# Performance work log

Measured on AMD Instinct MI355X. Metric: run time of the kernel, lower is better.

The kernel has to match this reference:

```python
import jax, jax.numpy as jnp
import numpy as np

P = 8          # patch_size = window_size // 3
C = 3          # in_channel (forced to 3 by the module's reshape logic)
QK_SCALE = 1.0


def _rel_bias(p):
    """Fixed relative-position bias [9, p, p], matching the torch constructor."""
    i = np.arange(p, dtype=np.float64)
    down = np.exp(-i / (p / 2))[:, None] * np.ones((1, p))   # down[i, :] = exp(-i/(p/2))
    right = down.T
    br = np.exp(-(i[:, None] + i[None, :]) / (p / 2))        # symmetric exp(-(i+j)/(p/2))
    merge = np.stack([
        np.rot90(br, 2), np.flip(down, 0), np.rot90(br, 1),
        np.flip(right, 1), np.ones((p, p)), right,
        np.rot90(br, 3), down, br,
    ], axis=0)
    return jnp.asarray(merge, dtype=jnp.float32)


def setup_inputs() -> dict:
    key = jax.random.key(0)
    k1, k2, k3 = jax.random.split(key, 3)
    b, c, h, w = 8, C, 512, 512
    d = c * P * P  # 192
    x = jax.random.normal(k1, (b, c, h, w), jnp.float32)
    W_qkv = jax.random.normal(k2, (3 * d, d), jnp.float32) * 0.05  # torch Linear weight [out, in]
    b_qkv = jax.random.normal(k3, (3 * d,), jnp.float32) * 0.01
    return {"x": x, "W_qkv": W_qkv, "b_qkv": b_qkv}


def reference(x, W_qkv, b_qkv):
    p, c = P, C
    b, _, h, w = x.shape
    nh, nw = h // p, w // p
    # pad by one patch on each side (zeros)
    xp = jnp.pad(x, ((0, 0), (0, 0), (p, p), (p, p)))
    # patch grid: [b, c, nh+2, p, nw+2, p] -> [b, nh+2, nw+2, c, p, p]
    g = xp.reshape(b, c, nh + 2, p, nw + 2, p).transpose(0, 2, 4, 1, 3, 5)
    # 9 neighbor patches per window, index k = 3*di + dj (row-major over 3x3 blocks)
    neigh = jnp.stack(
        [g[:, di:di + nh, dj:dj + nw] for di in range(3) for dj in range(3)],
        axis=3,
    )  # [b, nh, nw, 9, c, p, p]
    feat = neigh.reshape(b, nh, nw, 9, c * p * p)
    # qkv linear: y = feat @ W^T + b
    qkv = jnp.einsum('bijnd,ed->bijne', feat, W_qkv) + b_qkv  # [b, nh, nw, 9, 3*c*p*p]
    qkv = qkv.reshape(b, nh, nw, 9, 3, c, p, p)
    q = qkv[..., 0, :, :, :]  # [b, nh, nw, 9, c, p, p]
    k = qkv[..., 1, :, :, :]
    v = qkv[..., 2, :, :, :]
    core_q = q[:, :, :, 4] * QK_SCALE          # center patch query [b, nh, nw, c, p, p]
    bias = _rel_bias(p)                        # [9, p, p]
    # elementwise attention: (q * k * bias) * v, summed over the 9-neighbor window
    attn = core_q[:, :, :, None] * k * bias[:, None]   # [b, nh, nw, 9, c, p, p]
    out = jnp.sum(attn * v, axis=3)                    # [b, nh, nw, c, p, p]
    # reassemble to image: [b, c, nh, p, nw, p] -> [b, c, h, w]
    return out.transpose(0, 3, 1, 4, 2, 5).reshape(b, c, nh * p, nw * p)
```

## Files before the change

### kernel.cpp

```cpp
#include <hip/hip_runtime.h>


#define HW 512
#define PLANE 6291456

typedef __attribute__((ext_vector_type(8))) short bf16x8;
typedef __attribute__((ext_vector_type(4))) float f32x4;

static __device__ __forceinline__ unsigned short bf16_rne(float f) {
    unsigned u = __builtin_bit_cast(unsigned, f);
    u += 0x7FFFu + ((u >> 16) & 1u);
    return (unsigned short)(u >> 16);
}
static __device__ __forceinline__ float bf16f(unsigned short h) {
    unsigned u = ((unsigned)h) << 16;
    return __builtin_bit_cast(float, u);
}

__global__ void __launch_bounds__(256) xsplit_kernel(
    const float* __restrict__ x,
    unsigned short* __restrict__ xh,
    unsigned short* __restrict__ xl)
{
    int gid = blockIdx.x * 256 + threadIdx.x;
    const float4* s = (const float4*)x + (size_t)gid * 2;
    float4 a = s[0], b = s[1];
    float v[8] = {a.x, a.y, a.z, a.w, b.x, b.y, b.z, b.w};
    unsigned short h[8], lo[8];
    #pragma unroll
    for (int u = 0; u < 8; ++u) {
        h[u]  = bf16_rne(v[u]);
        lo[u] = bf16_rne(v[u] - bf16f(h[u]));
    }
    uint4 hp, lp;
    hp.x = (unsigned)h[0] | ((unsigned)h[1] << 16);
    hp.y = (unsigned)h[2] | ((unsigned)h[3] << 16);
    hp.z = (unsigned)h[4] | ((unsigned)h[5] << 16);
    hp.w = (unsigned)h[6] | ((unsigned)h[7] << 16);
    lp.x = (unsigned)lo[0] | ((unsigned)lo[1] << 16);
    lp.y = (unsigned)lo[2] | ((unsigned)lo[3] << 16);
    lp.z = (unsigned)lo[4] | ((unsigned)lo[5] << 16);
    lp.w = (unsigned)lo[6] | ((unsigned)lo[7] << 16);
    ((uint4*)xh)[gid] = hp;
    ((uint4*)xl)[gid] = lp;
}

__global__ void __launch_bounds__(256) wprep_kernel(const float* __restrict__ W,
                                                    unsigned short* __restrict__ Ws)
{
    int gid = blockIdx.x * 256 + threadIdx.x;
    int er  = gid % 192;
    int t   = gid / 192;
    int kg  = t & 7;
    int ckt = t >> 3;
    int c = ckt / 3, kt = ckt % 3;
    int slot = er >> 6, dl = er & 63;
    const float* src = W + (size_t)(slot*192 + c*64 + dl)*192 + kt*64 + kg*8;
    float4 a = ((const float4*)src)[0], b = ((const float4*)src)[1];
    float v[8] = {a.x, a.y, a.z, a.w, b.x, b.y, b.z, b.w};
    unsigned short h[8], lo[8];
    #pragma unroll
    for (int u = 0; u < 8; ++u) {
        h[u]  = bf16_rne(v[u]);
        lo[u] = bf16_rne(v[u] - bf16f(h[u]));
    }
    uint4 hp, lp;
    hp.x = (unsigned)h[0] | ((unsigned)h[1] << 16);
    hp.y = (unsigned)h[2] | ((unsigned)h[3] << 16);
    hp.z = (unsigned)h[4] | ((unsigned)h[5] << 16);
    hp.w = (unsigned)h[6] | ((unsigned)h[7] << 16);
    lp.x = (unsigned)lo[0] | ((unsigned)lo[1] << 16);
    lp.y = (unsigned)lo[2] | ((unsigned)lo[3] << 16);
    lp.z = (unsigned)lo[4] | ((unsigned)lo[5] << 16);
    lp.w = (unsigned)lo[6] | ((unsigned)lo[7] << 16);
    size_t oh = ((size_t)((ckt*2 + 0)*8 + kg)*192 + er) * 8;
    size_t ol = ((size_t)((ckt*2 + 1)*8 + kg)*192 + er) * 8;
    *(uint4*)(Ws + oh) = hp;
    *(uint4*)(Ws + ol) = lp;
}

__global__ void __launch_bounds__(256) qkv_mfma_kernel(
    const unsigned short* __restrict__ xh,
    const unsigned short* __restrict__ xl,
    const unsigned short* __restrict__ Ws,
    const float* __restrict__ bqkv,
    float* __restrict__ ws)
{
    const int tid = threadIdx.x;
    const int mb  = blockIdx.x;
    const int c   = blockIdx.y;
    const int b   = mb >> 6, i = mb & 63;
    const int wv  = tid >> 6;
    const int l   = tid & 63;
    const int lr  = l & 15;
    const int lk  = l >> 4;

    f32x4 acc[4][3];
    #pragma unroll
    for (int m = 0; m < 4; ++m)
        #pragma unroll
        for (int n = 0; n < 3; ++n)
            #pragma unroll
            for (int r = 0; r < 4; ++r) acc[m][n][r] = 0.f;

    #pragma unroll
    for (int kt = 0; kt < 3; ++kt) {
        const unsigned short* xhp = xh + ((size_t)(b*3 + kt)*HW + (size_t)i*8) * HW;
        const unsigned short* xlp = xl + ((size_t)(b*3 + kt)*HW + (size_t)i*8) * HW;
        const unsigned short* Bb  = Ws + (size_t)(c*3 + kt) * 2 * 8 * 192 * 8;
        #pragma unroll
        for (int ks = 0; ks < 2; ++ks) {
            const int pi = ks*4 + lk;
            bf16x8 ah[4], al[4];
            #pragma unroll
            for (int m = 0; m < 4; ++m) {
                int j = m*16 + lr;
                size_t o = (size_t)pi*HW + j*8;
                ah[m] = *(const bf16x8*)(xhp + o);
                al[m] = *(const bf16x8*)(xlp + o);
            }
            bf16x8 bh[3], bl[3];
            #pragma unroll
            for (int n = 0; n < 3; ++n) {
                int er = n*64 + wv*16 + lr;
                size_t oh = ((size_t)(0*8 + ks*4 + lk)*192 + er) * 8;
                size_t ol = ((size_t)(1*8 + ks*4 + lk)*192 + er) * 8;
                bh[n] = *(const bf16x8*)(Bb + oh);
                bl[n] = *(const bf16x8*)(Bb + ol);
            }
            #pragma unroll
            for (int m = 0; m < 4; ++m)
                #pragma unroll
                for (int n = 0; n < 3; ++n) {
                    acc[m][n] = __builtin_amdgcn_mfma_f32_16x16x32_bf16(al[m], bh[n], acc[m][n], 0, 0, 0);
                    acc[m][n] = __builtin_amdgcn_mfma_f32_16x16x32_bf16(ah[m], bl[n], acc[m][n], 0, 0, 0);
                    acc[m][n] = __builtin_amdgcn_mfma_f32_16x16x32_bf16(ah[m], bh[n], acc[m][n], 0, 0, 0);
                }
        }
    }

    const int dl = wv*16 + lr;
    const float bq = bqkv[      c*64 + dl];
    const float bk = bqkv[192 + c*64 + dl];
    const float bv = bqkv[384 + c*64 + dl];
    const int ppi = dl >> 3, ppj = dl & 7;
    float* qplane = ws;
    float* wplane = ws + PLANE;
    size_t rowoff = ((size_t)(b*3 + c)*HW + (size_t)(i*8 + ppi))*HW + ppj;
    #pragma unroll
    for (int m = 0; m < 4; ++m)
        #pragma unroll
        for (int ri = 0; ri < 4; ++ri) {
            int j = m*16 + lk*4 + ri;
            float qv = acc[m][0][ri] + bq;
            float wvv = (acc[m][1][ri] + bk) * (acc[m][2][ri] + bv);
            qplane[rowoff + (size_t)j*8] = qv;
            wplane[rowoff + (size_t)j*8] = wvv;
        }
}

__global__ void __launch_bounds__(256) attn_kernel(
    const float* __restrict__ ws,
    const float* __restrict__ bqkv,
    float* __restrict__ out)
{
    __shared__ float wt[80][84];
    const int tid = threadIdx.x;
    int bid = blockIdx.x;
    int txt = (bid & 7) << 6;
    int tyt = ((bid >> 3) & 7) << 6;
    int pl  = bid >> 6;
    int c   = pl % 3;
    const float* qplane = ws + (size_t)pl * (HW*HW);
    const float* wplane = ws + PLANE + (size_t)pl * (HW*HW);

    const int pi  = (tid >> 4) & 7;
    const int pj0 = (tid & 1) << 2;
    const float fr0 = __expf((float)(pi - 7) * 0.25f);
    const float fr2 = __expf((float)(-pi) * 0.25f);
    float fa[4], fb[4];
    #pragma unroll
    for (int u = 0; u < 4; ++u) {
        int pj = pj0 + u;
        fa[u] = __expf((float)(pj - 7) * 0.25f);
        fb[u] = __expf((float)(-pj) * 0.25f);
    }

    for (int it = 0; it < 7; ++it) {
        int f = tid + it*256;
        if (f < 1600) {
            int r  = f / 20;
            int c4 = f - r*20;
            int gy = tyt - 8 + r;
            int gx = txt - 8 + (c4 << 2);
            float4 v;
            if ((unsigned)gy < 512u && (unsigned)gx < 512u) {
                v = *(const float4*)(wplane + (size_t)gy*HW + gx);
            } else {
                int d0 = c*64 + (gy & 7)*8 + (gx & 7);
                float4 bk = *(const float4*)(bqkv + 192 + d0);
                float4 bv = *(const float4*)(bqkv + 384 + d0);
                v.x = bk.x*bv.x; v.y = bk.y*bv.y; v.z = bk.z*bv.z; v.w = bk.w*bv.w;
            }
            *(float4*)&wt[r][c4 << 2] = v;
        }
    }
    __syncthreads();

    #pragma unroll
    for (int it = 0; it < 4; ++it) {
        int f  = tid + it*256;
        int ly = f >> 4;
        int lx = (f & 15) << 2;
        float sx = 0.f, sy = 0.f, sz = 0.f, sw = 0.f;
        #pragma unroll
        for (int di = 0; di < 3; ++di) {
            const float* row = &wt[ly + 8*di][lx];
            float4 w0 = *(const float4*)(row);
            float4 w1 = *(const float4*)(row + 8);
            float4 w2 = *(const float4*)(row + 16);
            float fr = (di == 0) ? fr0 : (di == 1) ? 1.f : fr2;
            sx += fr * (fa[0]*w0.x + w1.x + fb[0]*w2.x);
            sy += fr * (fa[1]*w0.y + w1.y + fb[1]*w2.y);
            sz += fr * (fa[2]*w0.z + w1.z + fb[2]*w2.z);
            sw += fr * (fa[3]*w0.w + w1.w + fb[3]*w2.w);
        }
        size_t off = (size_t)pl*(HW*HW) + (size_t)(tyt + ly)*HW + txt + lx;
        float4 q4 = *(const float4*)(qplane + (size_t)(tyt + ly)*HW + txt + lx);
        float4 o;
        o.x = q4.x*sx; o.y = q4.y*sy; o.z = q4.z*sz; o.w = q4.w*sw;
        *(float4*)(out + off) = o;
    }
}

extern "C" void kernel_launch(void* const* d_in, const int* in_sizes, int n_in,
                              void* d_out, int out_size, void* d_ws, size_t ws_size,
                              hipStream_t stream)
{
    const float* x  = (const float*)d_in[0];
    const float* W  = (const float*)d_in[1];
    const float* bq = (const float*)d_in[2];
    float* wsf = (float*)d_ws;
    unsigned short* xh = (unsigned short*)(wsf + 2*(size_t)PLANE);
    unsigned short* xl = xh + PLANE;
    unsigned short* Wsplit = xl + PLANE;

    xsplit_kernel<<<3072, 256, 0, stream>>>(x, xh, xl);
    wprep_kernel<<<54, 256, 0, stream>>>(W, Wsplit);
    qkv_mfma_kernel<<<dim3(512, 3), 256, 0, stream>>>(xh, xl, Wsplit, bq, wsf);
    attn_kernel<<<1536, 256, 0, stream>>>(wsf, bq, (float*)d_out);
}
```

Before: 123.6 us.

## Fuse x split, QKV MFMA GEMM and attention into one tiled kernel

Replaces the separate x-split, QKV GEMM and attention kernels with one kernel per 64x64 tile and channel. It loads a haloed x tile, splits it to bf16 hi/lo in swizzled LDS, runs the MFMA GEMM on 100 patches including the halo, and keeps q and k*v in LDS for the attention stencil. This removes the global round trips for the bf16 copies of x and the q and k*v planes. In exchange it recomputes the GEMM for halo patches (100 versus 64 per tile), reads each x channel three times (once per output channel), and adds more LDS and synchronisation.

```diff
diff --git a/kernel.cpp b/kernel.cpp
--- a/kernel.cpp
+++ b/kernel.cpp
@@ -2,7 +2,6 @@
 
 
 #define HW 512
-#define PLANE 6291456
 
 typedef __attribute__((ext_vector_type(8))) short bf16x8;
 typedef __attribute__((ext_vector_type(4))) float f32x4;
@@ -17,14 +16,16 @@
     return __builtin_bit_cast(float, u);
 }
 
-__global__ void __launch_bounds__(256) xsplit_kernel(
-    const float* __restrict__ x,
-    unsigned short* __restrict__ xh,
-    unsigned short* __restrict__ xl)
+__global__ void __launch_bounds__(256) wprep_kernel(const float* __restrict__ W,
+                                                    unsigned short* __restrict__ Ws)
 {
     int gid = blockIdx.x * 256 + threadIdx.x;
-    const float4* s = (const float4*)x + (size_t)gid * 2;
-    float4 a = s[0], b = s[1];
+    int e  = gid % 576;
+    int t  = gid / 576;
+    int kg = t & 7;
+    int kt = t >> 3;
+    const float* src = W + (size_t)e*192 + kt*64 + kg*8;
+    float4 a = ((const float4*)src)[0], b = ((const float4*)src)[1];
     float v[8] = {a.x, a.y, a.z, a.w, b.x, b.y, b.z, b.w};
     unsigned short h[8], lo[8];
     #pragma unroll
@@ -41,195 +42,178 @@
     lp.y = (unsigned)lo[2] | ((unsigned)lo[3] << 16);
     lp.z = (unsigned)lo[4] | ((unsigned)lo[5] << 16);
     lp.w = (unsigned)lo[6] | ((unsigned)lo[7] << 16);
-    ((uint4*)xh)[gid] = hp;
-    ((uint4*)xl)[gid] = lp;
-}
-
-__global__ void __launch_bounds__(256) wprep_kernel(const float* __restrict__ W,
-                                                    unsigned short* __restrict__ Ws)
-{
-    int gid = blockIdx.x * 256 + threadIdx.x;
-    int er  = gid % 192;
-    int t   = gid / 192;
-    int kg  = t & 7;
-    int ckt = t >> 3;
-    int c = ckt / 3, kt = ckt % 3;
-    int slot = er >> 6, dl = er & 63;
-    const float* src = W + (size_t)(slot*192 + c*64 + dl)*192 + kt*64 + kg*8;
-    float4 a = ((const float4*)src)[0], b = ((const float4*)src)[1];
-    float v[8] = {a.x, a.y, a.z, a.w, b.x, b.y, b.z, b.w};
-    unsigned short h[8], lo[8];
-    #pragma unroll
-    for (int u = 0; u < 8; ++u) {
-        h[u]  = bf16_rne(v[u]);
-        lo[u] = bf16_rne(v[u] - bf16f(h[u]));
-    }
-    uint4 hp, lp;
-    hp.x = (unsigned)h[0] | ((unsigned)h[1] << 16);
-    hp.y = (unsigned)h[2] | ((unsigned)h[3] << 16);
-    hp.z = (unsigned)h[4] | ((unsigned)h[5] << 16);
-    hp.w = (unsigned)h[6] | ((unsigned)h[7] << 16);
-    lp.x = (unsigned)lo[0] | ((unsigned)lo[1] << 16);
-    lp.y = (unsigned)lo[2] | ((unsigned)lo[3] << 16);
-    lp.z = (unsigned)lo[4] | ((unsigned)lo[5] << 16);
-    lp.w = (unsigned)lo[6] | ((unsigned)lo[7] << 16);
-    size_t oh = ((size_t)((ckt*2 + 0)*8 + kg)*192 + er) * 8;
-    size_t ol = ((size_t)((ckt*2 + 1)*8 + kg)*192 + er) * 8;
+    size_t oh = ((((size_t)kt*2 + 0)*8 + kg)*576 + e) * 8;
+    size_t ol = ((((size_t)kt*2 + 1)*8 + kg)*576 + e) * 8;
     *(uint4*)(Ws + oh) = hp;
     *(uint4*)(Ws + ol) = lp;
 }
 
-__global__ void __launch_bounds__(256) qkv_mfma_kernel(
-    const unsigned short* __restrict__ xh,
-    const unsigned short* __restrict__ xl,
+__global__ void __launch_bounds__(512) fused_kernel(
+    const float* __restrict__ x,
     const unsigned short* __restrict__ Ws,
-    const float* __restrict__ bqkv,
-    float* __restrict__ ws)
-{
-    const int tid = threadIdx.x;
-    const int mb  = blockIdx.x;
-    const int c   = blockIdx.y;
-    const int b   = mb >> 6, i = mb & 63;
-    const int wv  = tid >> 6;
-    const int l   = tid & 63;
-    const int lr  = l & 15;
-    const int lk  = l >> 4;
-
-    f32x4 acc[4][3];
-    #pragma unroll
-    for (int m = 0; m < 4; ++m)
-        #pragma unroll
-        for (int n = 0; n < 3; ++n)
-            #pragma unroll
-            for (int r = 0; r < 4; ++r) acc[m][n][r] = 0.f;
-
-    #pragma unroll
-    for (int kt = 0; kt < 3; ++kt) {
-        const unsigned short* xhp = xh + ((size_t)(b*3 + kt)*HW + (size_t)i*8) * HW;
-        const unsigned short* xlp = xl + ((size_t)(b*3 + kt)*HW + (size_t)i*8) * HW;
-        const unsigned short* Bb  = Ws + (size_t)(c*3 + kt) * 2 * 8 * 192 * 8;
-        #pragma unroll
-        for (int ks = 0; ks < 2; ++ks) {
-            const int pi = ks*4 + lk;
-            bf16x8 ah[4], al[4];
-            #pragma unroll
-            for (int m = 0; m < 4; ++m) {
-                int j = m*16 + lr;
-                size_t o = (size_t)pi*HW + j*8;
-                ah[m] = *(const bf16x8*)(xhp + o);
-                al[m] = *(const bf16x8*)(xlp + o);
-            }
-            bf16x8 bh[3], bl[3];
-            #pragma unroll
-            for (int n = 0; n < 3; ++n) {
-                int er = n*64 + wv*16 + lr;
-                size_t oh = ((size_t)(0*8 + ks*4 + lk)*192 + er) * 8;
-                size_t ol = ((size_t)(1*8 + ks*4 + lk)*192 + er) * 8;
-                bh[n] = *(const bf16x8*)(Bb + oh);
-                bl[n] = *(const bf16x8*)(Bb + ol);
-            }
-            #pragma unroll
-            for (int m = 0; m < 4; ++m)
-                #pragma unroll
-                for (int n = 0; n < 3; ++n) {
-                    acc[m][n] = __builtin_amdgcn_mfma_f32_16x16x32_bf16(al[m], bh[n], acc[m][n], 0, 0, 0);
-                    acc[m][n] = __builtin_amdgcn_mfma_f32_16x16x32_bf16(ah[m], bl[n], acc[m][n], 0, 0, 0);
-                    acc[m][n] = __builtin_amdgcn_mfma_f32_16x16x32_bf16(ah[m], bh[n], acc[m][n], 0, 0, 0);
-                }
-        }
-    }
-
-    const int dl = wv*16 + lr;
-    const float bq = bqkv[      c*64 + dl];
-    const float bk = bqkv[192 + c*64 + dl];
-    const float bv = bqkv[384 + c*64 + dl];
-    const int ppi = dl >> 3, ppj = dl & 7;
-    float* qplane = ws;
-    float* wplane = ws + PLANE;
-    size_t rowoff = ((size_t)(b*3 + c)*HW + (size_t)(i*8 + ppi))*HW + ppj;
-    #pragma unroll
-    for (int m = 0; m < 4; ++m)
-        #pragma unroll
-        for (int ri = 0; ri < 4; ++ri) {
-            int j = m*16 + lk*4 + ri;
-            float qv = acc[m][0][ri] + bq;
-            float wvv = (acc[m][1][ri] + bk) * (acc[m][2][ri] + bv);
-            qplane[rowoff + (size_t)j*8] = qv;
-            wplane[rowoff + (size_t)j*8] = wvv;
-        }
-}
-
-__global__ void __launch_bounds__(256) attn_kernel(
-    const float* __restrict__ ws,
     const float* __restrict__ bqkv,
     float* __restrict__ out)
 {
-    __shared__ float wt[80][84];
+    __shared__ char smem[44608];
+    unsigned short* Ah = (unsigned short*)smem;
+    unsigned short* Al = (unsigned short*)(smem + 16384);
+    float* w_lds = (float*)smem;
+    float* q_lds = (float*)(smem + 27200);
+
     const int tid = threadIdx.x;
     int bid = blockIdx.x;
-    int txt = (bid & 7) << 6;
-    int tyt = ((bid >> 3) & 7) << 6;
-    int pl  = bid >> 6;
-    int c   = pl % 3;
-    const float* qplane = ws + (size_t)pl * (HW*HW);
-    const float* wplane = ws + PLANE + (size_t)pl * (HW*HW);
-
-    const int pi  = (tid >> 4) & 7;
-    const int pj0 = (tid & 1) << 2;
-    const float fr0 = __expf((float)(pi - 7) * 0.25f);
-    const float fr2 = __expf((float)(-pi) * 0.25f);
-    float fa[4], fb[4];
-    #pragma unroll
-    for (int u = 0; u < 4; ++u) {
-        int pj = pj0 + u;
-        fa[u] = __expf((float)(pj - 7) * 0.25f);
-        fb[u] = __expf((float)(-pj) * 0.25f);
-    }
-
-    for (int it = 0; it < 7; ++it) {
-        int f = tid + it*256;
-        if (f < 1600) {
-            int r  = f / 20;
-            int c4 = f - r*20;
-            int gy = tyt - 8 + r;
-            int gx = txt - 8 + (c4 << 2);
-            float4 v;
-            if ((unsigned)gy < 512u && (unsigned)gx < 512u) {
-                v = *(const float4*)(wplane + (size_t)gy*HW + gx);
-            } else {
-                int d0 = c*64 + (gy & 7)*8 + (gx & 7);
-                float4 bk = *(const float4*)(bqkv + 192 + d0);
-                float4 bv = *(const float4*)(bqkv + 384 + d0);
-                v.x = bk.x*bv.x; v.y = bk.y*bv.y; v.z = bk.z*bv.z; v.w = bk.w*bv.w;
-            }
-            *(float4*)&wt[r][c4 << 2] = v;
-        }
-    }
+    const int c  = bid % 3;
+    int t2 = bid / 3;
+    const int tx = t2 & 7;
+    const int ty = (t2 >> 3) & 7;
+    const int b  = t2 >> 6;
+
+    const int wv = tid >> 6;
+    const int l  = tid & 63;
+    const int lr = l & 15;
+    const int lk = l >> 4;
+    const int wm = wv >> 1;
+    const int wn = wv & 1;
+
+    f32x4 acc[2][6];
+    #pragma unroll
+    for (int mf = 0; mf < 2; ++mf)
+        #pragma unroll
+        for (int sp = 0; sp < 6; ++sp)
+            #pragma unroll
+            for (int r = 0; r < 4; ++r) acc[mf][sp][r] = 0.f;
+
+    const int gy0 = ty*64 - 8, gx0 = tx*64 - 8;
+
+    for (int kt = 0; kt < 3; ++kt) {
+        const float* xp = x + (size_t)(b*3 + kt) * HW * HW;
+        #pragma unroll
+        for (int it = 0; it < 4; ++it) {
+            int f = tid + it*512;
+            if (f < 1600) {
+                int r  = f / 20;
+                int c4 = f - r*20;
+                int gy = gy0 + r;
+                int gx = gx0 + c4*4;
+                float4 v = make_float4(0.f, 0.f, 0.f, 0.f);
+                if ((unsigned)gy < 512u && (unsigned)gx < 512u)
+                    v = *(const float4*)(xp + (size_t)gy*HW + gx);
+                int p  = (r >> 3)*10 + (c4 >> 1);
+                int kk = (r & 7)*8 + (c4 & 1)*4;
+                unsigned short h0 = bf16_rne(v.x), h1 = bf16_rne(v.y),
+                               h2 = bf16_rne(v.z), h3 = bf16_rne(v.w);
+                unsigned short q0 = bf16_rne(v.x - bf16f(h0)), q1 = bf16_rne(v.y - bf16f(h1)),
+                               q2 = bf16_rne(v.z - bf16f(h2)), q3 = bf16_rne(v.w - bf16f(h3));
+                int byte = (p*128 + kk*2) ^ ((p & 7) << 4);
+                *(uint2*)((char*)Ah + byte) = make_uint2((unsigned)h0 | ((unsigned)h1 << 16),
+                                                         (unsigned)h2 | ((unsigned)h3 << 16));
+                *(uint2*)((char*)Al + byte) = make_uint2((unsigned)q0 | ((unsigned)q1 << 16),
+                                                         (unsigned)q2 | ((unsigned)q3 << 16));
+            }
+        }
+        __syncthreads();
+
+        const unsigned short* Wk = Ws + (size_t)kt * 2 * 8 * 576 * 8;
+        #pragma unroll
+        for (int ks = 0; ks < 2; ++ks) {
+            bf16x8 ah[2], al[2];
+            #pragma unroll
+            for (int mf = 0; mf < 2; ++mf) {
+                int row = wm*32 + mf*16 + lr;
+                int byte = (row*128 + ks*64 + lk*16) ^ ((row & 7) << 4);
+                ah[mf] = *(const bf16x8*)((const char*)Ah + byte);
+                al[mf] = *(const bf16x8*)((const char*)Al + byte);
+            }
+            int kg = ks*4 + lk;
+            const unsigned short* Bh = Wk + (size_t)(0*8 + kg) * 576 * 8;
+            const unsigned short* Bl = Wk + (size_t)(1*8 + kg) * 576 * 8;
+            #pragma unroll
+            for (int sp = 0; sp < 6; ++sp) {
+                int slot = sp >> 1, nf2 = sp & 1;
+                int e = slot*192 + c*64 + wn*32 + nf2*16 + lr;
+                bf16x8 bh = *(const bf16x8*)(Bh + (size_t)e * 8);
+                bf16x8 bl = *(const bf16x8*)(Bl + (size_t)e * 8);
+                #pragma unroll
+                for (int mf = 0; mf < 2; ++mf) {
+                    acc[mf][sp] = __builtin_amdgcn_mfma_f32_16x16x32_bf16(al[mf], bh, acc[mf][sp], 0, 0, 0);
+                    acc[mf][sp] = __builtin_amdgcn_mfma_f32_16x16x32_bf16(ah[mf], bl, acc[mf][sp], 0, 0, 0);
+                    acc[mf][sp] = __builtin_amdgcn_mfma_f32_16x16x32_bf16(ah[mf], bh, acc[mf][sp], 0, 0, 0);
+                }
+            }
+        }
+        __syncthreads();
+    }
+
+    float bq[2], bk[2], bv[2];
+    #pragma unroll
+    for (int nf2 = 0; nf2 < 2; ++nf2) {
+        int dl = wn*32 + nf2*16 + lr;
+        bq[nf2] = bqkv[      c*64 + dl];
+        bk[nf2] = bqkv[192 + c*64 + dl];
+        bv[nf2] = bqkv[384 + c*64 + dl];
+    }
+    #pragma unroll
+    for (int mf = 0; mf < 2; ++mf)
+        #pragma unroll
+        for (int ri = 0; ri < 4; ++ri) {
+            int p = wm*32 + mf*16 + lk*4 + ri;
+            if (p < 100) {
+                #pragma unroll
+                for (int nf2 = 0; nf2 < 2; ++nf2) {
+                    int dl = wn*32 + nf2*16 + lr;
+                    float wval = (acc[mf][2 + nf2][ri] + bk[nf2]) * (acc[mf][4 + nf2][ri] + bv[nf2]);
+                    w_lds[p*68 + dl] = wval;
+                }
+                int pr = p / 10, pc = p - (p/10)*10;
+                if (pr >= 1 && pr <= 8 && pc >= 1 && pc <= 8) {
+                    int qi = (pr - 1)*8 + (pc - 1);
+                    #pragma unroll
+                    for (int nf2 = 0; nf2 < 2; ++nf2) {
+                        int dl = wn*32 + nf2*16 + lr;
+                        q_lds[qi*68 + dl] = acc[mf][nf2][ri] + bq[nf2];
+                    }
+                }
+            }
+        }
     __syncthreads();
 
     #pragma unroll
-    for (int it = 0; it < 4; ++it) {
-        int f  = tid + it*256;
-        int ly = f >> 4;
-        int lx = (f & 15) << 2;
+    for (int it = 0; it < 2; ++it) {
+        int e4  = tid + it*512;
+        int qi  = e4 >> 4;
+        int dlq = e4 & 15;
+        int dl0 = dlq << 2;
+        int pi  = dl0 >> 3;
+        int pj0 = dl0 & 7;
+        int p   = (1 + (qi >> 3))*10 + 1 + (qi & 7);
+        float fr0 = __expf((float)(pi - 7) * 0.25f);
+        float fr2 = __expf((float)(-pi) * 0.25f);
+        float fa[4], fb[4];
+        #pragma unroll
+        for (int u = 0; u < 4; ++u) {
+            int pj = pj0 + u;
+            fa[u] = __expf((float)(pj - 7) * 0.25f);
+            fb[u] = __expf((float)(-pj) * 0.25f);
+        }
         float sx = 0.f, sy = 0.f, sz = 0.f, sw = 0.f;
         #pragma unroll
         for (int di = 0; di < 3; ++di) {
-            const float* row = &wt[ly + 8*di][lx];
-            float4 w0 = *(const float4*)(row);
-            float4 w1 = *(const float4*)(row + 8);
-            float4 w2 = *(const float4*)(row + 16);
+            const float* rowp = w_lds + (p + (di - 1)*10)*68 + dl0;
+            float4 wl = *(const float4*)(rowp - 68);
+            float4 wc = *(const float4*)(rowp);
+            float4 wr = *(const float4*)(rowp + 68);
             float fr = (di == 0) ? fr0 : (di == 1) ? 1.f : fr2;
-            sx += fr * (fa[0]*w0.x + w1.x + fb[0]*w2.x);
-            sy += fr * (fa[1]*w0.y + w1.y + fb[1]*w2.y);
-            sz += fr * (fa[2]*w0.z + w1.z + fb[2]*w2.z);
-            sw += fr * (fa[3]*w0.w + w1.w + fb[3]*w2.w);
-        }
-        size_t off = (size_t)pl*(HW*HW) + (size_t)(tyt + ly)*HW + txt + lx;
-        float4 q4 = *(const float4*)(qplane + (size_t)(tyt + ly)*HW + txt + lx);
+            sx += fr * (fa[0]*wl.x + wc.x + fb[0]*wr.x);
+            sy += fr * (fa[1]*wl.y + wc.y + fb[1]*wr.y);
+            sz += fr * (fa[2]*wl.z + wc.z + fb[2]*wr.z);
+            sw += fr * (fa[3]*wl.w + wc.w + fb[3]*wr.w);
+        }
+        float4 q4 = *(const float4*)(q_lds + qi*68 + dl0);
+        int y = ty*64 + (qi >> 3)*8 + pi;
+        int xg = tx*64 + (qi & 7)*8 + pj0;
         float4 o;
         o.x = q4.x*sx; o.y = q4.y*sy; o.z = q4.z*sz; o.w = q4.w*sw;
-        *(float4*)(out + off) = o;
+        *(float4*)(out + ((size_t)(b*3 + c)*HW + y)*HW + xg) = o;
     }
 }
 
@@ -240,13 +224,8 @@
     const float* x  = (const float*)d_in[0];
     const float* W  = (const float*)d_in[1];
     const float* bq = (const float*)d_in[2];
-    float* wsf = (float*)d_ws;
-    unsigned short* xh = (unsigned short*)(wsf + 2*(size_t)PLANE);
-    unsigned short* xl = xh + PLANE;
-    unsigned short* Wsplit = xl + PLANE;
-
-    xsplit_kernel<<<3072, 256, 0, stream>>>(x, xh, xl);
-    wprep_kernel<<<54, 256, 0, stream>>>(W, Wsplit);
-    qkv_mfma_kernel<<<dim3(512, 3), 256, 0, stream>>>(xh, xl, Wsplit, bq, wsf);
-    attn_kernel<<<1536, 256, 0, stream>>>(wsf, bq, (float*)d_out);
-}
+    unsigned short* Ws = (unsigned short*)d_ws;
+
+    wprep_kernel<<<54, 256, 0, stream>>>(W, Ws);
+    fused_kernel<<<1536, 512, 0, stream>>>(x, Ws, bq, (float*)d_out);
+}
```

Result: slower. 147.2 us (+19.1%).
